# Optimization experiments

Measured on AMD Instinct MI355X. Metric: run time of the kernel, lower is better.

## Reference

```python
import jax, jax.numpy as jnp
import numpy as np

DIM = 1024
HEADS = 16
DIM_HEAD = DIM // HEADS  # 64
B, N = 4, 1024


def setup_inputs() -> dict:
    key = jax.random.key(0)
    ks = jax.random.split(key, 8)
    s = 1.0 / np.sqrt(DIM)
    inp = {
        "x": jax.random.normal(ks[0], (B, N, DIM), dtype=jnp.float32),
        # weights stored as [in, out] so y = x @ W (+ b), equivalent to torch Linear
        "Wq": jax.random.normal(ks[1], (DIM, DIM), dtype=jnp.float32) * s,
        "Wk": jax.random.normal(ks[2], (DIM, DIM), dtype=jnp.float32) * s,
        "Wv": jax.random.normal(ks[3], (DIM, DIM), dtype=jnp.float32) * s,
        "Wproj": jax.random.normal(ks[4], (DIM, DIM), dtype=jnp.float32) * s,
        "bproj": jnp.zeros((DIM,), dtype=jnp.float32),
        "Wpre": jax.random.normal(ks[5], (DIM, DIM), dtype=jnp.float32) * s,
        "bpre": jnp.zeros((DIM,), dtype=jnp.float32),
        # original init is -inf (non-runnable); use a finite trained value
        "pi": jnp.full((1,), 0.5, dtype=jnp.float32),
    }
    return inp


def reference(x, Wq, Wk, Wv, Wproj, bproj, Wpre, bpre, pi):
    b, n, c = x.shape
    h, dh = HEADS, DIM_HEAD
    residual = x
    # bias-logit path: Linear -> SiLU -> bmm with itself (dropout p=0 is identity)
    pre = jax.nn.silu(x @ Wpre + bpre)                       # [B,N,C]
    logits = jnp.einsum('bnc,bmc->bnm', pre, pre) / jnp.sqrt(jnp.float32(c))
    # QKV (x2 defaults to x)
    q = (x @ Wq).reshape(b, n, h, dh).transpose(0, 2, 1, 3)  # [B,H,N,Dh]
    k = (x @ Wk).reshape(b, n, h, dh).transpose(0, 2, 1, 3)
    v = (x @ Wv).reshape(b, n, h, dh).transpose(0, 2, 1, 3)
    score = jnp.einsum('bhnd,bhmd->bhnm', q, k) / jnp.sqrt(jnp.float32(dh))
    final_logits = pi[0] * logits[:, None, :, :] + score     # broadcast bias over heads
    attn = jax.nn.softmax(final_logits, axis=-1)
    out = jnp.einsum('bhnm,bhmd->bhnd', attn, v)             # [B,H,N,Dh]
    out = out.transpose(0, 2, 1, 3).reshape(b, n, h * dh)
    out = out @ Wproj + bproj
    return out + residual
```

## Files before the change

kernel.cpp:

```cpp
#include <hip/hip_runtime.h>

using bf16x8 = __attribute__((ext_vector_type(8))) short;
using v8bf   = __attribute__((ext_vector_type(8))) __bf16;
using f32x4  = __attribute__((ext_vector_type(4))) float;

typedef const __attribute__((address_space(1))) void GASV;
typedef __attribute__((address_space(3))) void LASV;

template <typename V>
__device__ __forceinline__ auto mfma_bf16_impl(V a, V b, f32x4 c, int)
    -> decltype(__builtin_amdgcn_mfma_f32_16x16x32_bf16(a, b, c, 0, 0, 0)) {
  return __builtin_amdgcn_mfma_f32_16x16x32_bf16(a, b, c, 0, 0, 0);
}
template <typename V>
__device__ __forceinline__ f32x4 mfma_bf16_impl(V a, V b, f32x4 c, long) {
  return __builtin_amdgcn_mfma_f32_16x16x32_bf16(
      __builtin_bit_cast(v8bf, a), __builtin_bit_cast(v8bf, b), c, 0, 0, 0);
}
__device__ __forceinline__ f32x4 MFMA(bf16x8 a, bf16x8 b, f32x4 c) {
  return mfma_bf16_impl(a, b, c, 0);
}

__device__ __forceinline__ void async_lds16(const void* g, void* l) {
  __builtin_amdgcn_global_load_lds((GASV*)g, (LASV*)l, 16, 0, 0);
}

__device__ __forceinline__ unsigned short f2bf(float x) {
  unsigned u = __float_as_uint(x);
  u = u + 0x7fffu + ((u >> 16) & 1u);
  return (unsigned short)(u >> 16);
}

#define LOG2E 1.4426950408889634f
#define SOFT_OFF 14.0f

__global__ __launch_bounds__(256) void k_prep(
    const float4* __restrict__ x, ushort4* __restrict__ xb,
    const float* __restrict__ w0, const float* __restrict__ w1,
    const float* __restrict__ w2, const float* __restrict__ w3,
    const float* __restrict__ w4, unsigned short* __restrict__ out) {
  const int bid = blockIdx.x, tid = threadIdx.x;
  if (bid < 4096) {
    const int i = bid * 256 + tid;
    float4 v = x[i];
    ushort4 p;
    p.x = f2bf(v.x); p.y = f2bf(v.y); p.z = f2bf(v.z); p.w = f2bf(v.w);
    xb[i] = p;
    return;
  }
  __shared__ float t[32][33];
  const int tb = bid - 4096;
  const int z = tb >> 10;
  const float* W = (z == 0) ? w0 : (z == 1) ? w1 : (z == 2) ? w2 : (z == 3) ? w3 : w4;
  const float sc = (z == 1) ? (LOG2E / 8.0f) : 1.0f;
  unsigned short* o = out + (size_t)z * (1u << 20);
  const int bx = (tb & 31) * 32, by = ((tb >> 5) & 31) * 32;
  const int tx = tid & 31, ty = tid >> 5;
#pragma unroll
  for (int i = 0; i < 4; ++i)
    t[ty + i * 8][tx] = W[(size_t)(by + ty + i * 8) * 1024 + bx + tx];
  __syncthreads();
#pragma unroll
  for (int i = 0; i < 4; ++i)
    o[(size_t)(bx + ty + i * 8) * 1024 + by + tx] = f2bf(t[tx][ty + i * 8] * sc);
}

template <int MI, int NI>
__device__ __forceinline__ void gemm_core_t(const unsigned short* __restrict__ A,
                                            const unsigned short* __restrict__ Bt,
                                            unsigned short* ldsA,
                                            unsigned short* ldsB,
                                            f32x4 acc[MI][NI]) {
  const int tid = threadIdx.x;
  const int w = tid >> 6, lane = tid & 63;
  const int lane15 = lane & 15, quad = lane >> 4;
  const int wm = w >> 1, wn = w & 1;
  for (int ko = 0; ko < 16; ++ko) {
    __syncthreads();
#pragma unroll
    for (int i = 0; i < MI; ++i) {
      const int p = i * 256 + tid;
      const int r = p >> 3, cc = (p & 7) ^ (r & 7);
      async_lds16(A + r * 1024 + ko * 64 + cc * 8, ldsA + (i * 256 + w * 64) * 8);
    }
#pragma unroll
    for (int i = 0; i < NI; ++i) {
      const int p = i * 256 + tid;
      const int r = p >> 3, cc = (p & 7) ^ (r & 7);
      async_lds16(Bt + r * 1024 + ko * 64 + cc * 8, ldsB + (i * 256 + w * 64) * 8);
    }
    __syncthreads();
    bf16x8 af[MI][2], bfr[NI][2];
#pragma unroll
    for (int t = 0; t < MI; ++t) {
      const int row = wm * (MI * 16) + t * 16 + lane15;
#pragma unroll
      for (int h = 0; h < 2; ++h)
        af[t][h] = *(const bf16x8*)&ldsA[row * 64 + (((h * 4 + quad) ^ (row & 7)) << 3)];
    }
#pragma unroll
    for (int t = 0; t < NI; ++t) {
      const int row = wn * (NI * 16) + t * 16 + lane15;
#pragma unroll
      for (int h = 0; h < 2; ++h)
        bfr[t][h] = *(const bf16x8*)&ldsB[row * 64 + (((h * 4 + quad) ^ (row & 7)) << 3)];
    }
#pragma unroll
    for (int mi = 0; mi < MI; ++mi)
#pragma unroll
      for (int ni = 0; ni < NI; ++ni) {
        acc[mi][ni] = MFMA(af[mi][0], bfr[ni][0], acc[mi][ni]);
        acc[mi][ni] = MFMA(af[mi][1], bfr[ni][1], acc[mi][ni]);
      }
  }
}

#define GEMM_PROLOGUE(MI_, NI_)                                      \
  __shared__ unsigned short ldsA[(MI_)*32 * 64];                     \
  __shared__ unsigned short ldsB[(NI_)*32 * 64];                     \
  f32x4 acc[MI_][NI_];                                               \
  {                                                                  \
    f32x4 z_ = {0.f, 0.f, 0.f, 0.f};                                 \
    for (int i_ = 0; i_ < (MI_); ++i_)                               \
      for (int j_ = 0; j_ < (NI_); ++j_) acc[i_][j_] = z_;           \
  }

#define GEMM_EPI_IDX(MI_, NI_)                                       \
  const int tid = threadIdx.x, w = tid >> 6, lane = tid & 63;        \
  const int lane15 = lane & 15, quad = lane >> 4;                    \
  const int wm = w >> 1, wn = w & 1;                                 \
  const int r0 = tm + wm * ((MI_)*16) + quad * 4;                    \
  const int c0 = tn + wn * ((NI_)*16) + lane15;

__global__ __launch_bounds__(256) void k_gemm_qkvpre(
    const unsigned short* __restrict__ xb, const unsigned short* __restrict__ wt,
    const float* __restrict__ bpre, unsigned short* __restrict__ pre,
    unsigned short* __restrict__ qb, unsigned short* __restrict__ kb,
    unsigned short* __restrict__ vt) {
  const int bid = blockIdx.x;
  const int xcd = bid & 7, idx = bid >> 3;
  const int z = xcd >> 1, half = xcd & 1;
  const int wtile = (idx >> 4) * 128;
  const int stile = half * 2048 + (idx & 15) * 128;
  int tm, tn;
  if (z == 3) { tm = stile; tn = wtile; }
  else        { tm = wtile; tn = stile; }
  const unsigned short* At =
      (z == 3) ? xb + (size_t)tm * 1024
               : wt + (size_t)z * (1u << 20) + (size_t)tm * 1024;
  const unsigned short* Bt_ =
      (z == 3) ? wt + (size_t)3 * (1u << 20) + (size_t)tn * 1024
               : xb + (size_t)tn * 1024;
  GEMM_PROLOGUE(4, 4);
  gemm_core_t<4, 4>(At, Bt_, ldsA, ldsB, acc);
  GEMM_EPI_IDX(4, 4);
  if (z == 0) {
#pragma unroll
    for (int mi = 0; mi < 4; ++mi) {
      const float4 b4 = *(const float4*)&bpre[r0 + mi * 16];
#pragma unroll
      for (int ni = 0; ni < 4; ++ni) {
        const int seq = c0 + ni * 16;
        float vv[4];
#pragma unroll
        for (int rr = 0; rr < 4; ++rr) {
          float v = acc[mi][ni][rr] + ((const float*)&b4)[rr];
          vv[rr] = v / (1.0f + __expf(-v));
        }
        ushort4 pk;
        pk.x = f2bf(vv[0]); pk.y = f2bf(vv[1]);
        pk.z = f2bf(vv[2]); pk.w = f2bf(vv[3]);
        *(ushort4*)&pre[(size_t)seq * 1024 + r0 + mi * 16] = pk;
      }
    }
  } else if (z == 1 || z == 2) {
    unsigned short* dst = (z == 1) ? qb : kb;
#pragma unroll
    for (int mi = 0; mi < 4; ++mi)
#pragma unroll
      for (int ni = 0; ni < 4; ++ni) {
        const int seq = c0 + ni * 16;
        ushort4 pk;
        pk.x = f2bf(acc[mi][ni][0]); pk.y = f2bf(acc[mi][ni][1]);
        pk.z = f2bf(acc[mi][ni][2]); pk.w = f2bf(acc[mi][ni][3]);
        *(ushort4*)&dst[(size_t)seq * 1024 + r0 + mi * 16] = pk;
      }
  } else {
#pragma unroll
    for (int mi = 0; mi < 4; ++mi) {
      const int m = r0 + mi * 16;
      const int bb_ = m >> 10, nseq = m & 1023;
#pragma unroll
      for (int ni = 0; ni < 4; ++ni) {
        const int cg = c0 + ni * 16;
        const int hh = cg >> 6, dd = cg & 63;
        ushort4 pk;
        pk.x = f2bf(acc[mi][ni][0]); pk.y = f2bf(acc[mi][ni][1]);
        pk.z = f2bf(acc[mi][ni][2]); pk.w = f2bf(acc[mi][ni][3]);
        *(ushort4*)&vt[(size_t)(((bb_ * 16 + hh) << 6) + dd) * 1024 + nseq] = pk;
      }
    }
  }
}

__global__ __launch_bounds__(256) void k_gemm_logits(
    const unsigned short* __restrict__ pre, const float* __restrict__ pi,
    unsigned short* __restrict__ lg) {
  const int bz = blockIdx.z;
  const unsigned short* base = pre + ((size_t)bz << 20);
  const int tm = blockIdx.y * 64, tn = blockIdx.x * 128;
  GEMM_PROLOGUE(2, 4);
  gemm_core_t<2, 4>(base + (size_t)tm * 1024, base + (size_t)tn * 1024, ldsA, ldsB, acc);
  const float sc = pi[0] * (LOG2E / 32.0f);
  GEMM_EPI_IDX(2, 4);
#pragma unroll
  for (int mi = 0; mi < 2; ++mi)
#pragma unroll
    for (int ni = 0; ni < 4; ++ni) {
      const int col = c0 + ni * 16;
      ushort4 pk;
      pk.x = f2bf(acc[mi][ni][0] * sc); pk.y = f2bf(acc[mi][ni][1] * sc);
      pk.z = f2bf(acc[mi][ni][2] * sc); pk.w = f2bf(acc[mi][ni][3] * sc);
      *(ushort4*)&lg[((size_t)bz << 20) + (size_t)col * 1024 + r0 + mi * 16] = pk;
    }
}

__global__ __launch_bounds__(256) void k_gemm_out(
    const unsigned short* __restrict__ ao, const unsigned short* __restrict__ wtp,
    const float* __restrict__ bproj, const float* __restrict__ xres,
    float* __restrict__ out) {
  const int tm = blockIdx.x * 64, tn = blockIdx.y * 128;
  GEMM_PROLOGUE(2, 4);
  gemm_core_t<2, 4>(wtp + (size_t)tm * 1024, ao + (size_t)tn * 1024, ldsA, ldsB, acc);
  GEMM_EPI_IDX(2, 4);
#pragma unroll
  for (int mi = 0; mi < 2; ++mi) {
    const float4 b4 = *(const float4*)&bproj[r0 + mi * 16];
#pragma unroll
    for (int ni = 0; ni < 4; ++ni) {
      const int seq = c0 + ni * 16;
      const size_t idx = (size_t)seq * 1024 + r0 + mi * 16;
      const float4 rv = *(const float4*)&xres[idx];
      float4 ov;
      ov.x = acc[mi][ni][0] + b4.x + rv.x;
      ov.y = acc[mi][ni][1] + b4.y + rv.y;
      ov.z = acc[mi][ni][2] + b4.z + rv.z;
      ov.w = acc[mi][ni][3] + b4.w + rv.w;
      *(float4*)&out[idx] = ov;
    }
  }
}

__global__ __launch_bounds__(256, 4) void k_attn(
    const unsigned short* __restrict__ qb, const unsigned short* __restrict__ kb,
    const unsigned short* __restrict__ vt, const unsigned short* __restrict__ lg,
    unsigned short* __restrict__ ao) {
  __shared__ unsigned short ldsK[2 * 64 * 64];
  __shared__ unsigned short ldsV[2 * 64 * 64];
  const int bid = blockIdx.x;
  const int xcd = bid & 7, idx = bid >> 3;
  const int b = xcd >> 1, hg = xcd & 1;
  const int h = hg * 8 + (idx >> 4);
  const int q0 = (idx & 15) * 64;
  const int tid = threadIdx.x, w = tid >> 6, lane = tid & 63;
  const int lane15 = lane & 15, quad = lane >> 4;
  const int qw = q0 + w * 16;
  const int src0 = (quad & 1) * 32 + lane15;
  const int src1 = src0 + 16;
  const bool hiq = quad >= 2;

  bf16x8 qf[2];
  {
    const unsigned short* qrow =
        qb + (size_t)((b << 10) + qw + lane15) * 1024 + (h << 6);
    qf[0] = *(const bf16x8*)(qrow + quad * 8);
    qf[1] = *(const bf16x8*)(qrow + 32 + quad * 8);
  }
  const unsigned short* kbase = kb + ((size_t)(b << 10)) * 1024 + (h << 6);
  const unsigned short* vbase = vt + ((size_t)((b * 16 + h) << 6)) * 1024;
  const unsigned short* lgrow =
      lg + ((size_t)b << 20) + (size_t)(qw + lane15) * 1024 + quad * 4;

  float lcol = 0.f;
  f32x4 o[4];
  {
    f32x4 z_ = {0.f, 0.f, 0.f, 0.f};
#pragma unroll
    for (int nt = 0; nt < 4; ++nt) o[nt] = z_;
  }

  uint2 lgc[4], lgn[4];

  auto stage = [&](int ch, unsigned short* sK, unsigned short* sV) {
    const int kv0 = ch * 64;
#pragma unroll
    for (int i = 0; i < 2; ++i) {
      const int p = i * 256 + tid;
      const int r = p >> 3, cc = (p & 7) ^ (r & 7);
      async_lds16(kbase + (size_t)(kv0 + r) * 1024 + cc * 8,
                  sK + (i * 256 + w * 64) * 8);
      async_lds16(vbase + (size_t)r * 1024 + kv0 + cc * 8,
                  sV + (i * 256 + w * 64) * 8);
    }
  };
  auto lgload = [&](int ch, uint2 dst[4]) {
#pragma unroll
    for (int mi = 0; mi < 4; ++mi)
      dst[mi] = *(const uint2*)(lgrow + ch * 64 + mi * 16);
  };
  auto compute = [&](const unsigned short* sK, const unsigned short* sV) {
    f32x4 s[4];
    __builtin_amdgcn_s_setprio(1);
#pragma unroll
    for (int mi = 0; mi < 4; ++mi) {
      const int row = mi * 16 + lane15;
      bf16x8 k0 = *(const bf16x8*)&sK[row * 64 + ((quad ^ (row & 7)) << 3)];
      bf16x8 k1 = *(const bf16x8*)&sK[row * 64 + (((4 + quad) ^ (row & 7)) << 3)];
      f32x4 t;
      t[0] = __uint_as_float(lgc[mi].x << 16);
      t[1] = __uint_as_float(lgc[mi].x & 0xffff0000u);
      t[2] = __uint_as_float(lgc[mi].y << 16);
      t[3] = __uint_as_float(lgc[mi].y & 0xffff0000u);
      t = MFMA(k0, qf[0], t);
      t = MFMA(k1, qf[1], t);
      s[mi] = t;
    }
    __builtin_amdgcn_s_setprio(0);
    float rs = 0.f;
    uint2 pk[4];
#pragma unroll
    for (int mi = 0; mi < 4; ++mi) {
      const float p0 = exp2f(s[mi][0] - SOFT_OFF), p1 = exp2f(s[mi][1] - SOFT_OFF);
      const float p2 = exp2f(s[mi][2] - SOFT_OFF), p3 = exp2f(s[mi][3] - SOFT_OFF);
      rs += (p0 + p1) + (p2 + p3);
      pk[mi].x = ((__float_as_uint(p1) + 0x8000u) & 0xffff0000u) |
                 ((__float_as_uint(p0) + 0x8000u) >> 16);
      pk[mi].y = ((__float_as_uint(p3) + 0x8000u) & 0xffff0000u) |
                 ((__float_as_uint(p2) + 0x8000u) >> 16);
    }
    lcol += rs;

#pragma unroll
    for (int kp = 0; kp < 2; ++kp) {
      const unsigned x0a = __shfl(pk[2 * kp].x, src0);
      const unsigned y0a = __shfl(pk[2 * kp].y, src0);
      const unsigned x1a = __shfl(pk[2 * kp].x, src1);
      const unsigned y1a = __shfl(pk[2 * kp].y, src1);
      const unsigned x0b = __shfl(pk[2 * kp + 1].x, src0);
      const unsigned y0b = __shfl(pk[2 * kp + 1].y, src0);
      const unsigned x1b = __shfl(pk[2 * kp + 1].x, src1);
      const unsigned y1b = __shfl(pk[2 * kp + 1].y, src1);
      uint4 bfv;
      bfv.x = hiq ? x0b : x0a;
      bfv.y = hiq ? y0b : y0a;
      bfv.z = hiq ? x1b : x1a;
      bfv.w = hiq ? y1b : y1a;
      const bf16x8 pf = __builtin_bit_cast(bf16x8, bfv);
      __builtin_amdgcn_s_setprio(1);
#pragma unroll
      for (int dt = 0; dt < 4; ++dt) {
        const int d = dt * 16 + lane15;
        bf16x8 vf = *(const bf16x8*)&sV[d * 64 +
                                        (((kp * 4 + quad) ^ (d & 7)) << 3)];
        o[dt] = MFMA(vf, pf, o[dt]);
      }
      __builtin_amdgcn_s_setprio(0);
    }
  };

  unsigned short* sK0 = ldsK;
  unsigned short* sK1 = ldsK + 64 * 64;
  unsigned short* sV0 = ldsV;
  unsigned short* sV1 = ldsV + 64 * 64;

  stage(0, sK0, sV0);
  lgload(0, lgc);
  __syncthreads();

  for (int c = 0; c < 16; c += 2) {
    stage(c + 1, sK1, sV1);
    lgload(c + 1, lgn);
    compute(sK0, sV0);
    __syncthreads();
#pragma unroll
    for (int mi = 0; mi < 4; ++mi) lgc[mi] = lgn[mi];
    if (c + 2 < 16) {
      stage(c + 2, sK0, sV0);
      lgload(c + 2, lgn);
    }
    compute(sK1, sV1);
    __syncthreads();
#pragma unroll
    for (int mi = 0; mi < 4; ++mi) lgc[mi] = lgn[mi];
  }

  lcol += __shfl_xor(lcol, 16);
  lcol += __shfl_xor(lcol, 32);
  const float rinv = 1.0f / lcol;
  const int m = (b << 10) + qw + lane15;
#pragma unroll
  for (int dt = 0; dt < 4; ++dt) {
    ushort4 pkk;
    pkk.x = f2bf(o[dt][0] * rinv);
    pkk.y = f2bf(o[dt][1] * rinv);
    pkk.z = f2bf(o[dt][2] * rinv);
    pkk.w = f2bf(o[dt][3] * rinv);
    *(ushort4*)&ao[(size_t)m * 1024 + (h << 6) + dt * 16 + quad * 4] = pkk;
  }
}

extern "C" void kernel_launch(void* const* d_in, const int* in_sizes, int n_in,
                              void* d_out, int out_size, void* d_ws, size_t ws_size,
                              hipStream_t stream) {
  const float* x     = (const float*)d_in[0];
  const float* Wq    = (const float*)d_in[1];
  const float* Wk    = (const float*)d_in[2];
  const float* Wv    = (const float*)d_in[3];
  const float* Wproj = (const float*)d_in[4];
  const float* bproj = (const float*)d_in[5];
  const float* Wpre  = (const float*)d_in[6];
  const float* bpre  = (const float*)d_in[7];
  const float* pi    = (const float*)d_in[8];
  float* out = (float*)d_out;
  char* ws = (char*)d_ws;

  unsigned short* xb  = (unsigned short*)(ws);
  unsigned short* wt  = (unsigned short*)(ws + (8u << 20));
  unsigned short* pre = (unsigned short*)(ws + (18u << 20));
  unsigned short* qb  = (unsigned short*)(ws + (26u << 20));
  unsigned short* kb  = (unsigned short*)(ws + (34u << 20));
  unsigned short* vt  = (unsigned short*)(ws + (42u << 20));
  unsigned short* lg  = xb;
  unsigned short* ao  = pre;

  k_prep<<<dim3(4096 + 5120), dim3(256), 0, stream>>>(
      (const float4*)x, (ushort4*)xb, Wpre, Wq, Wk, Wv, Wproj, wt);
  k_gemm_qkvpre<<<dim3(1024), dim3(256), 0, stream>>>(xb, wt, bpre, pre, qb, kb, vt);
  k_gemm_logits<<<dim3(8, 16, 4), dim3(256), 0, stream>>>(pre, pi, lg);
  k_attn<<<dim3(1024), dim3(256), 0, stream>>>(qb, kb, vt, lg, ao);
  k_gemm_out<<<dim3(16, 32, 1), dim3(256), 0, stream>>>(ao, wt + 4 * (1u << 20), bproj, x, out);
}
```

Measured before the change: 224.2 us.

## Retile fused QKV/pre GEMM to 256x256 blocks with double-buffered LDS

Rewrites the fused QKV+pre projection GEMM so each 512-thread block computes a 256x256 tile instead of 128x128, with an explicit double-buffered async global-to-LDS pipeline, XOR-swizzled LDS layout, and MFMA priority hints. Larger tiles cut global/L2 traffic per FLOP and overlap loads with compute. The cost is 128 KB of LDS per block and 128 accumulator floats per thread, which lowers occupancy. The grid also drops to 256 blocks, which may underfill the GPU's compute units.

New measurement: 216.7 us. 1.03x faster.

```diff
diff --git a/kernel.cpp b/kernel.cpp
--- a/kernel.cpp
+++ b/kernel.cpp
@@ -132,16 +132,18 @@
   const int r0 = tm + wm * ((MI_)*16) + quad * 4;                    \
   const int c0 = tn + wn * ((NI_)*16) + lane15;
 
-__global__ __launch_bounds__(256) void k_gemm_qkvpre(
+__global__ __launch_bounds__(512, 2) void k_gemm_qkvpre(
     const unsigned short* __restrict__ xb, const unsigned short* __restrict__ wt,
     const float* __restrict__ bpre, unsigned short* __restrict__ pre,
     unsigned short* __restrict__ qb, unsigned short* __restrict__ kb,
     unsigned short* __restrict__ vt) {
+  __shared__ unsigned short ldsA[2][256 * 64];
+  __shared__ unsigned short ldsB[2][256 * 64];
   const int bid = blockIdx.x;
   const int xcd = bid & 7, idx = bid >> 3;
   const int z = xcd >> 1, half = xcd & 1;
-  const int wtile = (idx >> 4) * 128;
-  const int stile = half * 2048 + (idx & 15) * 128;
+  const int wtile = (idx >> 3) * 256;
+  const int stile = half * 2048 + (idx & 7) * 256;
   int tm, tn;
   if (z == 3) { tm = stile; tn = wtile; }
   else        { tm = wtile; tn = stile; }
@@ -151,52 +153,120 @@
   const unsigned short* Bt_ =
       (z == 3) ? wt + (size_t)3 * (1u << 20) + (size_t)tn * 1024
                : xb + (size_t)tn * 1024;
-  GEMM_PROLOGUE(4, 4);
-  gemm_core_t<4, 4>(At, Bt_, ldsA, ldsB, acc);
-  GEMM_EPI_IDX(4, 4);
+
+  const int tid = threadIdx.x, w = tid >> 6, lane = tid & 63;
+  const int lane15 = lane & 15, quad = lane >> 4;
+  const int wm = w >> 2, wn = w & 3;
+
+  f32x4 acc[8][4];
+  {
+    f32x4 z_ = {0.f, 0.f, 0.f, 0.f};
+#pragma unroll
+    for (int i = 0; i < 8; ++i)
+#pragma unroll
+      for (int j = 0; j < 4; ++j) acc[i][j] = z_;
+  }
+
+  auto stage = [&](int ko, int buf) {
+#pragma unroll
+    for (int j = 0; j < 4; ++j) {
+      const int p = j * 512 + tid;
+      const int r = p >> 3, cc = (p & 7) ^ (r & 7);
+      async_lds16(At + (size_t)r * 1024 + ko * 64 + cc * 8,
+                  &ldsA[buf][(j * 512 + w * 64) * 8]);
+      async_lds16(Bt_ + (size_t)r * 1024 + ko * 64 + cc * 8,
+                  &ldsB[buf][(j * 512 + w * 64) * 8]);
+    }
+  };
+
+  auto compute = [&](int buf) {
+    const unsigned short* sA = ldsA[buf];
+    const unsigned short* sB = ldsB[buf];
+    bf16x8 bfr[4][2];
+#pragma unroll
+    for (int nf = 0; nf < 4; ++nf) {
+      const int row = wn * 64 + nf * 16 + lane15;
+#pragma unroll
+      for (int kh = 0; kh < 2; ++kh)
+        bfr[nf][kh] =
+            *(const bf16x8*)&sB[row * 64 + (((kh * 4 + quad) ^ (row & 7)) << 3)];
+    }
+#pragma unroll
+    for (int mp = 0; mp < 4; ++mp) {
+      bf16x8 af[2][2];
+#pragma unroll
+      for (int i = 0; i < 2; ++i) {
+        const int row = wm * 128 + (mp * 2 + i) * 16 + lane15;
+#pragma unroll
+        for (int kh = 0; kh < 2; ++kh)
+          af[i][kh] =
+              *(const bf16x8*)&sA[row * 64 + (((kh * 4 + quad) ^ (row & 7)) << 3)];
+      }
+      __builtin_amdgcn_s_setprio(1);
+#pragma unroll
+      for (int i = 0; i < 2; ++i)
+#pragma unroll
+        for (int nf = 0; nf < 4; ++nf) {
+          acc[mp * 2 + i][nf] = MFMA(af[i][0], bfr[nf][0], acc[mp * 2 + i][nf]);
+          acc[mp * 2 + i][nf] = MFMA(af[i][1], bfr[nf][1], acc[mp * 2 + i][nf]);
+        }
+      __builtin_amdgcn_s_setprio(0);
+    }
+  };
+
+  stage(0, 0);
+  __syncthreads();
+  for (int t = 0; t < 16; ++t) {
+    if (t + 1 < 16) stage(t + 1, (t + 1) & 1);
+    compute(t & 1);
+    __syncthreads();
+  }
+
+  const int r0 = tm + wm * 128 + quad * 4;
+  const int c0 = tn + wn * 64 + lane15;
   if (z == 0) {
 #pragma unroll
-    for (int mi = 0; mi < 4; ++mi) {
-      const float4 b4 = *(const float4*)&bpre[r0 + mi * 16];
-#pragma unroll
-      for (int ni = 0; ni < 4; ++ni) {
-        const int seq = c0 + ni * 16;
+    for (int mf = 0; mf < 8; ++mf) {
+      const float4 b4 = *(const float4*)&bpre[r0 + mf * 16];
+#pragma unroll
+      for (int nf = 0; nf < 4; ++nf) {
+        const int seq = c0 + nf * 16;
         float vv[4];
 #pragma unroll
         for (int rr = 0; rr < 4; ++rr) {
-          float v = acc[mi][ni][rr] + ((const float*)&b4)[rr];
+          float v = acc[mf][nf][rr] + ((const float*)&b4)[rr];
           vv[rr] = v / (1.0f + __expf(-v));
         }
         ushort4 pk;
         pk.x = f2bf(vv[0]); pk.y = f2bf(vv[1]);
         pk.z = f2bf(vv[2]); pk.w = f2bf(vv[3]);
-        *(ushort4*)&pre[(size_t)seq * 1024 + r0 + mi * 16] = pk;
+        *(ushort4*)&pre[(size_t)seq * 1024 + r0 + mf * 16] = pk;
       }
     }
   } else if (z == 1 || z == 2) {
     unsigned short* dst = (z == 1) ? qb : kb;
 #pragma unroll
-    for (int mi = 0; mi < 4; ++mi)
-#pragma unroll
-      for (int ni = 0; ni < 4; ++ni) {
-        const int seq = c0 + ni * 16;
+    for (int mf = 0; mf < 8; ++mf)
+#pragma unroll
+      for (int nf = 0; nf < 4; ++nf) {
+        const int seq = c0 + nf * 16;
         ushort4 pk;
-        pk.x = f2bf(acc[mi][ni][0]); pk.y = f2bf(acc[mi][ni][1]);
-        pk.z = f2bf(acc[mi][ni][2]); pk.w = f2bf(acc[mi][ni][3]);
-        *(ushort4*)&dst[(size_t)seq * 1024 + r0 + mi * 16] = pk;
+        pk.x = f2bf(acc[mf][nf][0]); pk.y = f2bf(acc[mf][nf][1]);
+        pk.z = f2bf(acc[mf][nf][2]); pk.w = f2bf(acc[mf][nf][3]);
+        *(ushort4*)&dst[(size_t)seq * 1024 + r0 + mf * 16] = pk;
       }
   } else {
 #pragma unroll
-    for (int mi = 0; mi < 4; ++mi) {
-      const int m = r0 + mi * 16;
+    for (int mf = 0; mf < 8; ++mf) {
+      const int m = r0 + mf * 16;
       const int bb_ = m >> 10, nseq = m & 1023;
 #pragma unroll
-      for (int ni = 0; ni < 4; ++ni) {
-        const int cg = c0 + ni * 16;
+      for (int nf = 0; nf < 4; ++nf) {
+        const int cg = c0 + nf * 16;
         const int hh = cg >> 6, dd = cg & 63;
         ushort4 pk;
-        pk.x = f2bf(acc[mi][ni][0]); pk.y = f2bf(acc[mi][ni][1]);
-        pk.z = f2bf(acc[mi][ni][2]); pk.w = f2bf(acc[mi][ni][3]);
+        pk.x = f2bf(acc[mf][nf][0]); pk.y = f2bf(acc[mf][nf][1]);
+        pk.z = f2bf(acc[mf][nf][2]); pk.w = f2bf(acc[mf][nf][3]);
         *(ushort4*)&vt[(size_t)(((bb_ * 16 + hh) << 6) + dd) * 1024 + nseq] = pk;
       }
     }
@@ -435,7 +505,7 @@
 
   k_prep<<<dim3(4096 + 5120), dim3(256), 0, stream>>>(
       (const float4*)x, (ushort4*)xb, Wpre, Wq, Wk, Wv, Wproj, wt);
-  k_gemm_qkvpre<<<dim3(1024), dim3(256), 0, stream>>>(xb, wt, bpre, pre, qb, kb, vt);
+  k_gemm_qkvpre<<<dim3(256), dim3(512), 0, stream>>>(xb, wt, bpre, pre, qb, kb, vt);
   k_gemm_logits<<<dim3(8, 16, 4), dim3(256), 0, stream>>>(pre, pi, lg);
   k_attn<<<dim3(1024), dim3(256), 0, stream>>>(qb, kb, vt, lg, ao);
   k_gemm_out<<<dim3(16, 32, 1), dim3(256), 0, stream>>>(ao, wt + 4 * (1u << 20), bproj, x, out);
```
